# Kernel tuning notes

Hardware: AMD Instinct MI355X
Metric: run time of the kernel (lower is better)

## Reference

```python
import jax, jax.numpy as jnp
import numpy as np
from itertools import combinations

N_QUBITS = 8
PAIRS = list(combinations(range(N_QUBITS), 2))  # 28 qubit pairs -> 28 features/node

# qubit 0 = first tensor factor (most significant bit of the basis index)
CNOT01 = jnp.array([[1,0,0,0],[0,1,0,0],[0,0,0,1],[0,0,1,0]], dtype=jnp.complex64)  # control q0, target q1
CNOT10 = jnp.array([[1,0,0,0],[0,0,0,1],[0,0,1,0],[0,1,0,0]], dtype=jnp.complex64)  # control q1, target q0
I2 = jnp.eye(2, dtype=jnp.complex64)
HZ = jnp.array([1.0, -1.0, 1.0, -1.0], dtype=jnp.complex64)  # diag(I kron Z)


def _rx(t):
    c = jnp.cos(t / 2).astype(jnp.complex64)
    s = jnp.sin(t / 2).astype(jnp.complex64)
    return jnp.stack([jnp.stack([c, -1j * s]), jnp.stack([-1j * s, c])])


def _ry(t):
    c = jnp.cos(t / 2).astype(jnp.complex64)
    s = jnp.sin(t / 2).astype(jnp.complex64)
    return jnp.stack([jnp.stack([c, -s]), jnp.stack([s, c])])


def _rz(t):
    e = jnp.exp(-0.5j * t.astype(jnp.complex64))
    z = jnp.zeros((), jnp.complex64)
    return jnp.stack([jnp.stack([e, z]), jnp.stack([z, jnp.conj(e)])])


def _pair_unitary(p):  # p: [6] params for one qubit pair
    A = _rz(p[5]) @ _ry(p[4]) @ _rx(p[3]) @ _rz(p[2]) @ _ry(p[1]) @ _rx(p[0])
    return CNOT01 @ (CNOT10 @ jnp.kron(A, I2))  # [4,4]


def _quantum_features(x, qweight):
    """Batched version of the per-node amplitude encoding + 28 two-qubit circuits."""
    N = x.shape[0]
    psi = (x / jnp.linalg.norm(x, axis=1, keepdims=True)).astype(jnp.complex64)  # [N,256]
    psi8 = psi.reshape((N,) + (2,) * N_QUBITS)
    Us = jax.vmap(_pair_unitary)(qweight.reshape(len(PAIRS), 6))  # [28,4,4]
    cols = []
    for p, (a, b) in enumerate(PAIRS):
        perm = (0, 1 + a, 1 + b) + tuple(1 + q for q in range(N_QUBITS) if q not in (a, b))
        v = jnp.transpose(psi8, perm).reshape(N, 4, 2 ** (N_QUBITS - 2))  # [N,4,64]
        rho = jnp.einsum('nim,njm->nij', v, jnp.conj(v))  # reduced 2-qubit DM [N,4,4]
        U = Us[p]
        # <I kron Z> after U rho U^dagger, mapped to [0,1]
        e = jnp.einsum('a,ab,nbc,ac->n', HZ, U, rho, jnp.conj(U))
        cols.append((jnp.real(e) + 1.0) * 0.5)
    return jnp.stack(cols, axis=1).astype(jnp.float32)  # [N,28]


def reference(x, edge_index, qweight, W1, b1, W2, b2):
    N = x.shape[0]
    x_deal = _quantum_features(x, qweight)  # [N,28]
    # gcn_norm with added self loops, edge_weight = 1
    loop = jnp.arange(N)
    src = jnp.concatenate([edge_index[0], loop])
    dst = jnp.concatenate([edge_index[1], loop])
    w = jnp.ones(src.shape[0], dtype=jnp.float32)
    deg = jax.ops.segment_sum(w, dst, num_segments=N)
    dinv = jax.lax.rsqrt(jnp.maximum(deg, 1e-12))
    norm = dinv[src] * w * dinv[dst]
    out = jax.ops.segment_sum(norm[:, None] * x_deal[src], dst, num_segments=N)  # [N,28]
    out = jax.nn.relu(out)
    g = (out.T @ out).reshape(1, 28 * 28)  # [1,784]
    h = jax.nn.relu(g @ W1.T + b1)
    return jax.nn.sigmoid(h @ W2.T + b2)  # [1,1]


def setup_inputs() -> dict:
    N, F, E = 50000, 256, 1600000
    key = jax.random.key(0)
    ks = jax.random.split(key, 6)
    x = jax.random.normal(ks[0], (N, F), dtype=jnp.float32)
    edge_index = jax.random.randint(ks[1], (2, E), 0, N, dtype=jnp.int64)
    qweight = jax.random.uniform(ks[2], (168,), dtype=jnp.float32) * (2.0 * np.pi)
    W1 = jax.random.normal(ks[3], (128, 784), dtype=jnp.float32) * 0.03
    b1 = jnp.zeros((128,), dtype=jnp.float32)
    W2 = jax.random.normal(ks[4], (1, 128), dtype=jnp.float32) * 0.08
    b2 = jnp.zeros((1,), dtype=jnp.float32)
    return {"x": x, "edge_index": edge_index, "qweight": qweight,
            "W1": W1, "b1": b1, "W2": W2, "b2": b2}
```

## Files before the change

kernel.cpp:

```cpp
#include <hip/hip_runtime.h>
#include <hip/hip_fp16.h>
#include <math.h>

#define N_NODES 50000
#define N_EDGES 1600000
#define BSHIFT 6
#define NB_BUCKETS 782
#define PART_CHUNK 8192
#define NCHUNK 196
#define CAP 3072
#define ZSTRIDE 32
#define GREP 16

template<int CTRL>
__device__ inline float dpp_mov(float x){
    return __int_as_float(__builtin_amdgcn_update_dpp(0, __float_as_int(x), CTRL, 0xf, 0xf, false));
}
__device__ inline float wave_sum_dpp(float x){
    x += dpp_mov<0x111>(x);
    x += dpp_mov<0x112>(x);
    x += dpp_mov<0x114>(x);
    x += dpp_mov<0x118>(x);
    x += dpp_mov<0x142>(x);
    x += dpp_mov<0x143>(x);
    return x;
}
__device__ inline float lane63(float x){
    return __int_as_float(__builtin_amdgcn_readlane(__float_as_int(x), 63));
}
#define DPP_XOR1 0xB1
#define DPP_XOR2 0x4E

struct C2 { float x, y; };
__device__ inline C2 mkc(float x, float y){ C2 r; r.x=x; r.y=y; return r; }
__device__ inline C2 cmul(C2 a, C2 b){ return mkc(a.x*b.x - a.y*b.y, a.x*b.y + a.y*b.x); }
__device__ inline C2 cadd(C2 a, C2 b){ return mkc(a.x+b.x, a.y+b.y); }

__global__ __launch_bounds__(256) void k_init(const float* __restrict__ qw,
        const void* __restrict__ ei, float4* __restrict__ cmat,
        int* __restrict__ flag, int* __restrict__ bucketFill, float* __restrict__ G){
    int t = threadIdx.x;
    for (int i = t; i < NB_BUCKETS; i += 256) bucketFill[i] = 0;
    for (int i = t; i < GREP*784; i += 256) G[i] = 0.f;
    if (t == 255){
        const long long* e64 = (const long long*)ei;
        int ok = 1;
        for (int i = 0; i < 64; i++){
            long long v = e64[i];
            if (v < 0 || v >= N_NODES) ok = 0;
        }
        flag[0] = ok;
    }
    if (t < 28){
        int p = t;
        int a = 0; { int rem = p, q = 0; while (rem >= 7 - q){ rem -= 7 - q; q++; } a = q; }
        C2 M00 = mkc(1,0), M01 = mkc(0,0), M10 = mkc(0,0), M11 = mkc(1,0);
        for (int k = 0; k < 6; k++){
            float th = 0.5f * qw[p*6 + k];
            float s, c; sincosf(th, &s, &c);
            C2 R00, R01, R10, R11;
            int type = k % 3;
            if (type == 0){
                R00 = mkc(c,0); R01 = mkc(0,-s); R10 = mkc(0,-s); R11 = mkc(c,0);
            } else if (type == 1){
                R00 = mkc(c,0); R01 = mkc(-s,0); R10 = mkc(s,0); R11 = mkc(c,0);
            } else {
                R00 = mkc(c,-s); R01 = mkc(0,0); R10 = mkc(0,0); R11 = mkc(c,s);
            }
            C2 N00 = cadd(cmul(R00,M00), cmul(R01,M10));
            C2 N01 = cadd(cmul(R00,M01), cmul(R01,M11));
            C2 N10 = cadd(cmul(R10,M00), cmul(R11,M10));
            C2 N11 = cadd(cmul(R10,M01), cmul(R11,M11));
            M00=N00; M01=N01; M10=N10; M11=N11;
        }
        float B00  = (M00.x*M00.x + M00.y*M00.y) - (M10.x*M10.x + M10.y*M10.y);
        float B11  = (M01.x*M01.x + M01.y*M01.y) - (M11.x*M11.x + M11.y*M11.y);
        float B01r = (M00.x*M01.x + M00.y*M01.y) - (M10.x*M11.x + M10.y*M11.y);
        cmat[p] = make_float4(0.5f + 0.5f*B11, 0.5f*(B00 - B11), B01r, (float)a);
    }
}

__device__ inline int get_edge(const void* ei, int is64, long long idx){
    if (is64) return (int)((const long long*)ei)[idx];
    return ((const int*)ei)[idx];
}

__global__ __launch_bounds__(1024) void k_part(const void* __restrict__ ei,
        const int* __restrict__ flag, int* __restrict__ bucketFill,
        unsigned* __restrict__ pairs){
    __shared__ int hist[NB_BUCKETS];
    __shared__ int cntb[NB_BUCKETS];
    __shared__ int cursor[NB_BUCKETS];
    __shared__ int copyBase[NB_BUCKETS];
    __shared__ unsigned sorted[PART_CHUNK];
    int tid = threadIdx.x, c = blockIdx.x;
    long long base = (long long)c * PART_CHUNK;
    int cnt = (int)((N_EDGES - base < PART_CHUNK) ? (N_EDGES - base) : PART_CHUNK);
    int is64 = flag[0];
    unsigned ds[8], sr[8];
    #pragma unroll
    for (int k = 0; k < 8; k++){
        int i = tid + 1024*k;
        if (i < cnt){
            ds[k] = (unsigned)get_edge(ei, is64, (long long)N_EDGES + base + i);
            sr[k] = (unsigned)get_edge(ei, is64, base + i);
        } else ds[k] = 0xffffffffu;
    }
    if (tid < NB_BUCKETS) hist[tid] = 0;
    __syncthreads();
    #pragma unroll
    for (int k = 0; k < 8; k++)
        if (ds[k] != 0xffffffffu) atomicAdd(&hist[ds[k] >> BSHIFT], 1);
    __syncthreads();
    if (tid < NB_BUCKETS) cntb[tid] = hist[tid];
    __syncthreads();
    for (int ofs = 1; ofs < NB_BUCKETS; ofs <<= 1){
        int v = 0; bool a = tid < NB_BUCKETS;
        if (a) v = hist[tid] + (tid >= ofs ? hist[tid - ofs] : 0);
        __syncthreads();
        if (a) hist[tid] = v;
        __syncthreads();
    }
    if (tid < NB_BUCKETS){
        int cb = cntb[tid];
        int ls = hist[tid] - cb;
        int gbase = tid*CAP + atomicAdd(&bucketFill[tid], cb);
        copyBase[tid] = gbase - ls;
        cursor[tid] = ls;
    }
    __syncthreads();
    #pragma unroll
    for (int k = 0; k < 8; k++){
        if (ds[k] != 0xffffffffu){
            int pos = atomicAdd(&cursor[ds[k] >> BSHIFT], 1);
            sorted[pos] = (ds[k] << 16) | sr[k];
        }
    }
    __syncthreads();
    for (int i = tid; i < cnt; i += 1024){
        unsigned v = sorted[i];
        int b = (int)(v >> 22);
        pairs[copyBase[b] + i] = v;
    }
}

__global__ __launch_bounds__(256) void k_sort(const unsigned* __restrict__ pairs,
        const int* __restrict__ bucketFill, unsigned short* __restrict__ csr,
        int* __restrict__ nodeOff, float* __restrict__ dinv){
    __shared__ unsigned short sorted[CAP];
    __shared__ int hist[64];
    __shared__ int cursor[64];
    int b = blockIdx.x, t = threadIdx.x;
    int s0 = b*CAP;
    int cnt = bucketFill[b];
    if (cnt > CAP) cnt = CAP;
    if (t < 64) hist[t] = 0;
    __syncthreads();
    for (int i = t; i < cnt; i += 256){
        unsigned v = pairs[s0 + i];
        atomicAdd(&hist[(v >> 16) & 63], 1);
    }
    __syncthreads();
    int mycnt = (t < 64) ? hist[t] : 0;
    for (int ofs = 1; ofs < 64; ofs <<= 1){
        int nv = 0;
        if (t < 64) nv = hist[t] + (t >= ofs ? hist[t - ofs] : 0);
        __syncthreads();
        if (t < 64) hist[t] = nv;
        __syncthreads();
    }
    if (t < 64){
        cursor[t] = hist[t] - mycnt;
        int n = b*64 + t;
        if (n < N_NODES){
            nodeOff[n] = s0 + hist[t] - mycnt;
            dinv[n] = rsqrtf((float)(mycnt + 1));
        }
    }
    __syncthreads();
    for (int i = t; i < cnt; i += 256){
        unsigned v = pairs[s0 + i];
        int d = (v >> 16) & 63;
        int pos = atomicAdd(&cursor[d], 1);
        sorted[pos] = (unsigned short)(v & 0xffffu);
    }
    __syncthreads();
    for (int i = t; i < cnt; i += 256) csr[s0 + i] = sorted[i];
}

__global__ __launch_bounds__(256) void k_feat(const float* __restrict__ x,
        const float* __restrict__ dinv, const float4* __restrict__ cmat,
        __half* __restrict__ z){
    int wave = threadIdx.x >> 6;
    int lane = threadIdx.x & 63;
    int n = blockIdx.x*4 + wave;
    const float4 v = ((const float4*)(x + (size_t)n*256))[lane];
    float persq = v.x*v.x + v.y*v.y + v.z*v.z + v.w*v.w;

    float red[15];
    red[0] = persq;
    red[1] = v.x*v.x + v.y*v.y;
    red[2] = v.x*v.z + v.y*v.w;
    {
        float px = dpp_mov<DPP_XOR1>(v.x), py = dpp_mov<DPP_XOR1>(v.y);
        float pz = dpp_mov<DPP_XOR1>(v.z), pw = dpp_mov<DPP_XOR1>(v.w);
        red[3] = v.x*px + v.y*py + v.z*pz + v.w*pw;
        red[9] = (lane & 1) ? 0.f : persq;
    }
    {
        float px = dpp_mov<DPP_XOR2>(v.x), py = dpp_mov<DPP_XOR2>(v.y);
        float pz = dpp_mov<DPP_XOR2>(v.z), pw = dpp_mov<DPP_XOR2>(v.w);
        red[4] = v.x*px + v.y*py + v.z*pz + v.w*pw;
        red[10] = (lane & 2) ? 0.f : persq;
    }
    #pragma unroll
    for (int j = 2; j < 6; j++){
        float px = __shfl_xor(v.x, 1 << j), py = __shfl_xor(v.y, 1 << j);
        float pz = __shfl_xor(v.z, 1 << j), pw = __shfl_xor(v.w, 1 << j);
        red[3 + j] = v.x*px + v.y*py + v.z*pz + v.w*pw;
        red[9 + j] = ((lane >> j) & 1) ? 0.0f : persq;
    }
    float S[15];
    #pragma unroll
    for (int k = 0; k < 15; k++) S[k] = lane63(wave_sum_dpp(red[k]));

    if (lane < 28){
        float4 cm = cmat[lane];
        int ap = (int)cm.w;
        float S0a = (ap==6) ? S[1] :
                    (ap==0 ? S[14] : ap==1 ? S[13] : ap==2 ? S[12] :
                     ap==3 ? S[11] : ap==4 ? S[10] : S[9]);
        float Xa  = (ap==6) ? S[2] :
                    0.5f*(ap==0 ? S[8] : ap==1 ? S[7] : ap==2 ? S[6] :
                          ap==3 ? S[5] : ap==4 ? S[4] : S[3]);
        float feat = cm.x + (cm.y*S0a + cm.z*Xa) / S[0];
        z[(size_t)n*ZSTRIDE + lane] = __float2half(dinv[n] * feat);
    } else if (lane < 32){
        z[(size_t)n*ZSTRIDE + lane] = __float2half(0.f);
    }
}

__device__ inline void acc_pack(unsigned u, float& a, float& b){
    float2 f = __half22float2(__builtin_bit_cast(__half2, u));
    a += f.x; b += f.y;
}
__device__ inline void acc_row(const uint4* rp, float* acc ){
    uint4 w0 = rp[0], w1 = rp[1], w2 = rp[2], w3 = rp[3];
    acc_pack(w0.x, acc[0],  acc[1]);  acc_pack(w0.y, acc[2],  acc[3]);
    acc_pack(w0.z, acc[4],  acc[5]);  acc_pack(w0.w, acc[6],  acc[7]);
    acc_pack(w1.x, acc[8],  acc[9]);  acc_pack(w1.y, acc[10], acc[11]);
    acc_pack(w1.z, acc[12], acc[13]); acc_pack(w1.w, acc[14], acc[15]);
    acc_pack(w2.x, acc[16], acc[17]); acc_pack(w2.y, acc[18], acc[19]);
    acc_pack(w2.z, acc[20], acc[21]); acc_pack(w2.w, acc[22], acc[23]);
    acc_pack(w3.x, acc[24], acc[25]); acc_pack(w3.y, acc[26], acc[27]);
    acc_pack(w3.z, acc[28], acc[29]); acc_pack(w3.w, acc[30], acc[31]);
}

__global__ __launch_bounds__(256) void k_gather(const unsigned short* __restrict__ csr,
        const int* __restrict__ nodeOff, const int* __restrict__ bucketFill,
        const __half* __restrict__ z, const float* __restrict__ dinv,
        float* __restrict__ G){
    __shared__ float srow[64*28];
    int t = threadIdx.x;
    int n = blockIdx.x*64 + (t >> 2), sub = t & 3;
    bool valid = n < N_NODES;
    float acc[32];
    #pragma unroll
    for (int k = 0; k < 32; k++) acc[k] = 0.f;
    if (valid){
        int b = n >> 6, d = n & 63;
        int beg = nodeOff[n];
        int end = (d == 63 || n == N_NODES - 1) ? b*CAP + min(bucketFill[b], CAP)
                                                : nodeOff[n + 1];
        for (int i = beg + sub; i < end; i += 4){
            int src = csr[i];
            acc_row((const uint4*)(z + (size_t)src*ZSTRIDE), acc);
        }
        if (sub == 3) acc_row((const uint4*)(z + (size_t)n*ZSTRIDE), acc);
    }
    #pragma unroll
    for (int k = 0; k < 32; k++){
        acc[k] += dpp_mov<DPP_XOR1>(acc[k]);
        acc[k] += dpp_mov<DPP_XOR2>(acc[k]);
    }
    if (sub == 0){
        float dv = valid ? dinv[n] : 0.f;
        int d = (t >> 2);
        #pragma unroll
        for (int k = 0; k < 28; k++)
            srow[d*28 + k] = fmaxf(acc[k]*dv, 0.f);
    }
    __syncthreads();

    if (t < 196){
        float* Gr = G + (size_t)(blockIdx.x & (GREP-1)) * 784;
        int ti = t / 14, tj = t % 14;
        int i0 = 2*ti, j0 = 2*tj;
        float c00 = 0.f, c01 = 0.f, c10 = 0.f, c11 = 0.f;
        for (int nn = 0; nn < 64; nn++){
            const float* r = srow + nn*28;
            float a0 = r[i0], a1 = r[i0+1], b0 = r[j0], b1 = r[j0+1];
            c00 += a0*b0; c01 += a0*b1; c10 += a1*b0; c11 += a1*b1;
        }
        atomicAdd(&Gr[(i0  )*28 + j0  ], c00);
        atomicAdd(&Gr[(i0  )*28 + j0+1], c01);
        atomicAdd(&Gr[(i0+1)*28 + j0  ], c10);
        atomicAdd(&Gr[(i0+1)*28 + j0+1], c11);
    }
}

__global__ __launch_bounds__(256) void k_mlp(const float* __restrict__ G,
        const float* __restrict__ W1, const float* __restrict__ b1,
        const float* __restrict__ W2, const float* __restrict__ b2,
        float* __restrict__ outp){
    __shared__ float Gs[784];
    __shared__ float part[256];
    __shared__ float h[128];
    int t = threadIdx.x;
    for (int i = t; i < 784; i += 256){
        float s = 0.f;
        #pragma unroll
        for (int r = 0; r < GREP; r++) s += G[r*784 + i];
        Gs[i] = s;
    }
    __syncthreads();
    int j = t & 127, halfsel = t >> 7;
    const float* w = W1 + (size_t)j*784 + halfsel*392;
    const float* g = Gs + halfsel*392;
    float s = 0.f;
    for (int i = 0; i < 392; i++) s += g[i] * w[i];
    part[t] = s;
    __syncthreads();
    if (t < 128) h[t] = fmaxf(part[t] + part[t+128] + b1[t], 0.f) * W2[t];
    __syncthreads();
    for (int ofs = 64; ofs > 0; ofs >>= 1){
        if (t < ofs) h[t] += h[t + ofs];
        __syncthreads();
    }
    if (t == 0) outp[0] = 1.f / (1.f + expf(-(h[0] + b2[0])));
}

extern "C" void kernel_launch(void* const* d_in, const int* in_sizes, int n_in,
                              void* d_out, int out_size, void* d_ws, size_t ws_size,
                              hipStream_t stream){
    const float* x  = (const float*)d_in[0];
    const void*  ei = d_in[1];
    const float* qw = (const float*)d_in[2];
    const float* W1 = (const float*)d_in[3];
    const float* b1 = (const float*)d_in[4];
    const float* W2 = (const float*)d_in[5];
    const float* b2 = (const float*)d_in[6];
    float* outp = (float*)d_out;

    char* base = (char*)d_ws;
    __half*         z     = (__half*)base;         base += (size_t)N_NODES*ZSTRIDE*2;
    unsigned*       pairs = (unsigned*)base;       base += (size_t)NB_BUCKETS*CAP*4;
    unsigned short* csr   = (unsigned short*)base; base += (size_t)NB_BUCKETS*CAP*2;
    int*            nodeOff = (int*)base;          base += (size_t)N_NODES*4;
    float*          dinv  = (float*)base;          base += (size_t)N_NODES*4;
    float4*         cmat  = (float4*)base;         base += 448;
    float*          G     = (float*)base;          base += GREP*784*4;
    int*            bucketFill = (int*)base;       base += 4096;
    int*            flag  = (int*)base;            base += 16;

    k_init<<<1, 256, 0, stream>>>(qw, ei, cmat, flag, bucketFill, G);
    k_part<<<NCHUNK, 1024, 0, stream>>>(ei, flag, bucketFill, pairs);
    k_sort<<<NB_BUCKETS, 256, 0, stream>>>(pairs, bucketFill, csr, nodeOff, dinv);
    k_feat<<<N_NODES/4, 256, 0, stream>>>(x, dinv, cmat, z);
    k_gather<<<NB_BUCKETS, 256, 0, stream>>>(csr, nodeOff, bucketFill, z, dinv, G);
    k_mlp<<<1, 256, 0, stream>>>(G, W1, b1, W2, b2, outp);
}
```

Before: 180.5 us.

## Fuse per-bucket sort into gather kernel, keep CSR in shared memory

The bucket sort is moved from its own kernel into the gather kernel, so the sorted source indices stay in LDS instead of being written to and reread from a global CSR array with node offsets. A slim degree-only kernel still computes dinv before feature computation. The gather kernel now runs 512 threads with 8 lanes per node, adding a shuffle step to the reduction. The cost is that the pairs array is read twice (degree pass plus fused sort) and the gather blocks carry more LDS and sort work before they start loading features.

Result: faster. 176.4 us (-2.3%).

```diff
diff --git a/kernel.cpp b/kernel.cpp
--- a/kernel.cpp
+++ b/kernel.cpp
@@ -144,48 +144,22 @@
     }
 }
 
-__global__ __launch_bounds__(256) void k_sort(const unsigned* __restrict__ pairs,
-        const int* __restrict__ bucketFill, unsigned short* __restrict__ csr,
-        int* __restrict__ nodeOff, float* __restrict__ dinv){
-    __shared__ unsigned short sorted[CAP];
+__global__ __launch_bounds__(256) void k_deg(const unsigned* __restrict__ pairs,
+        const int* __restrict__ bucketFill, float* __restrict__ dinv){
     __shared__ int hist[64];
-    __shared__ int cursor[64];
     int b = blockIdx.x, t = threadIdx.x;
     int s0 = b*CAP;
     int cnt = bucketFill[b];
     if (cnt > CAP) cnt = CAP;
     if (t < 64) hist[t] = 0;
     __syncthreads();
-    for (int i = t; i < cnt; i += 256){
-        unsigned v = pairs[s0 + i];
-        atomicAdd(&hist[(v >> 16) & 63], 1);
-    }
-    __syncthreads();
-    int mycnt = (t < 64) ? hist[t] : 0;
-    for (int ofs = 1; ofs < 64; ofs <<= 1){
-        int nv = 0;
-        if (t < 64) nv = hist[t] + (t >= ofs ? hist[t - ofs] : 0);
-        __syncthreads();
-        if (t < 64) hist[t] = nv;
-        __syncthreads();
-    }
+    for (int i = t; i < cnt; i += 256)
+        atomicAdd(&hist[(pairs[s0 + i] >> 16) & 63], 1);
+    __syncthreads();
     if (t < 64){
-        cursor[t] = hist[t] - mycnt;
         int n = b*64 + t;
-        if (n < N_NODES){
-            nodeOff[n] = s0 + hist[t] - mycnt;
-            dinv[n] = rsqrtf((float)(mycnt + 1));
-        }
-    }
-    __syncthreads();
-    for (int i = t; i < cnt; i += 256){
-        unsigned v = pairs[s0 + i];
-        int d = (v >> 16) & 63;
-        int pos = atomicAdd(&cursor[d], 1);
-        sorted[pos] = (unsigned short)(v & 0xffffu);
-    }
-    __syncthreads();
-    for (int i = t; i < cnt; i += 256) csr[s0 + i] = sorted[i];
+        if (n < N_NODES) dinv[n] = rsqrtf((float)(hist[t] + 1));
+    }
 }
 
 __global__ __launch_bounds__(256) void k_feat(const float* __restrict__ x,
@@ -256,36 +230,70 @@
     acc_pack(w3.z, acc[28], acc[29]); acc_pack(w3.w, acc[30], acc[31]);
 }
 
-__global__ __launch_bounds__(256) void k_gather(const unsigned short* __restrict__ csr,
-        const int* __restrict__ nodeOff, const int* __restrict__ bucketFill,
-        const __half* __restrict__ z, const float* __restrict__ dinv,
-        float* __restrict__ G){
+__global__ __launch_bounds__(512) void k_bucket(const unsigned* __restrict__ pairs,
+        const int* __restrict__ bucketFill, const __half* __restrict__ z,
+        const float* __restrict__ dinv, float* __restrict__ G){
+    __shared__ unsigned short sorted[CAP];
+    __shared__ int hist[64];
+    __shared__ int cursor[64];
+    __shared__ int begs[64];
+    __shared__ int cnts[64];
     __shared__ float srow[64*28];
-    int t = threadIdx.x;
-    int n = blockIdx.x*64 + (t >> 2), sub = t & 3;
+    int b = blockIdx.x, t = threadIdx.x;
+    int s0 = b*CAP;
+    int cnt = bucketFill[b];
+    if (cnt > CAP) cnt = CAP;
+    if (t < 64) hist[t] = 0;
+    __syncthreads();
+    for (int i = t; i < cnt; i += 512){
+        unsigned v = pairs[s0 + i];
+        atomicAdd(&hist[(v >> 16) & 63], 1);
+    }
+    __syncthreads();
+    int mycnt = (t < 64) ? hist[t] : 0;
+    for (int ofs = 1; ofs < 64; ofs <<= 1){
+        int nv = 0;
+        if (t < 64) nv = hist[t] + (t >= ofs ? hist[t - ofs] : 0);
+        __syncthreads();
+        if (t < 64) hist[t] = nv;
+        __syncthreads();
+    }
+    if (t < 64){
+        cursor[t] = hist[t] - mycnt;
+        begs[t]   = hist[t] - mycnt;
+        cnts[t]   = mycnt;
+    }
+    __syncthreads();
+    for (int i = t; i < cnt; i += 512){
+        unsigned v = pairs[s0 + i];
+        int d = (v >> 16) & 63;
+        int pos = atomicAdd(&cursor[d], 1);
+        sorted[pos] = (unsigned short)(v & 0xffffu);
+    }
+    __syncthreads();
+
+    int d = t >> 3, sub = t & 7;
+    int n = b*64 + d;
     bool valid = n < N_NODES;
     float acc[32];
     #pragma unroll
     for (int k = 0; k < 32; k++) acc[k] = 0.f;
     if (valid){
-        int b = n >> 6, d = n & 63;
-        int beg = nodeOff[n];
-        int end = (d == 63 || n == N_NODES - 1) ? b*CAP + min(bucketFill[b], CAP)
-                                                : nodeOff[n + 1];
-        for (int i = beg + sub; i < end; i += 4){
-            int src = csr[i];
+        int beg = begs[d], end = beg + cnts[d];
+        for (int i = beg + sub; i < end; i += 8){
+            int src = sorted[i];
             acc_row((const uint4*)(z + (size_t)src*ZSTRIDE), acc);
         }
-        if (sub == 3) acc_row((const uint4*)(z + (size_t)n*ZSTRIDE), acc);
+        if (sub == 7) acc_row((const uint4*)(z + (size_t)n*ZSTRIDE), acc);
     }
     #pragma unroll
     for (int k = 0; k < 32; k++){
         acc[k] += dpp_mov<DPP_XOR1>(acc[k]);
         acc[k] += dpp_mov<DPP_XOR2>(acc[k]);
+        acc[k] += __shfl_xor(acc[k], 4);
     }
     if (sub == 0){
         float dv = valid ? dinv[n] : 0.f;
-        int d = (t >> 2);
         #pragma unroll
         for (int k = 0; k < 28; k++)
             srow[d*28 + k] = fmaxf(acc[k]*dv, 0.f);
@@ -355,8 +363,6 @@
     char* base = (char*)d_ws;
     __half*         z     = (__half*)base;         base += (size_t)N_NODES*ZSTRIDE*2;
     unsigned*       pairs = (unsigned*)base;       base += (size_t)NB_BUCKETS*CAP*4;
-    unsigned short* csr   = (unsigned short*)base; base += (size_t)NB_BUCKETS*CAP*2;
-    int*            nodeOff = (int*)base;          base += (size_t)N_NODES*4;
     float*          dinv  = (float*)base;          base += (size_t)N_NODES*4;
     float4*         cmat  = (float4*)base;         base += 448;
     float*          G     = (float*)base;          base += GREP*784*4;
@@ -365,8 +371,8 @@
 
     k_init<<<1, 256, 0, stream>>>(qw, ei, cmat, flag, bucketFill, G);
     k_part<<<NCHUNK, 1024, 0, stream>>>(ei, flag, bucketFill, pairs);
-    k_sort<<<NB_BUCKETS, 256, 0, stream>>>(pairs, bucketFill, csr, nodeOff, dinv);
+    k_deg<<<NB_BUCKETS, 256, 0, stream>>>(pairs, bucketFill, dinv);
     k_feat<<<N_NODES/4, 256, 0, stream>>>(x, dinv, cmat, z);
-    k_gather<<<NB_BUCKETS, 256, 0, stream>>>(csr, nodeOff, bucketFill, z, dinv, G);
+    k_bucket<<<NB_BUCKETS, 512, 0, stream>>>(pairs, bucketFill, z, dinv, G);
     k_mlp<<<1, 256, 0, stream>>>(G, W1, b1, W2, b2, outp);
 }
```
